# Kernel optimization log

Hardware: AMD Instinct MI355X
Metric: run time of the kernel (lower is better)

The kernel has to match this reference:

```python
import jax, jax.numpy as jnp
import numpy as np

N_ATOMS = 100000
N_EDGES = 800000
ATOM_FDIM = 133
HIDDEN = 256
DEPTH = 3
NUM_MOLS = 4096
BN_EPS = 1e-5


def setup_inputs() -> dict:
    key = jax.random.key(0)
    ks = jax.random.split(key, 16)
    f_atoms = jax.random.normal(ks[0], (N_ATOMS, ATOM_FDIM), dtype=jnp.float32)
    edge_index = jax.random.randint(ks[1], (2, N_EDGES), 0, N_ATOMS, dtype=jnp.int64)
    segment_ids = jnp.sort(jax.random.randint(ks[2], (N_ATOMS,), 0, NUM_MOLS, dtype=jnp.int64))
    s = 1.0 / np.sqrt(HIDDEN)
    return {
        "f_atoms": f_atoms,
        "W_in_w": jax.random.normal(ks[3], (ATOM_FDIM, HIDDEN), dtype=jnp.float32) / np.sqrt(ATOM_FDIM),
        "W_in_b": jnp.zeros((HIDDEN,), dtype=jnp.float32),
        "w1": jax.random.normal(ks[4], (DEPTH, HIDDEN, HIDDEN), dtype=jnp.float32) * s,
        "b1": jnp.zeros((DEPTH, HIDDEN), dtype=jnp.float32),
        "g1": jnp.ones((DEPTH, HIDDEN), dtype=jnp.float32),
        "be1": jnp.zeros((DEPTH, HIDDEN), dtype=jnp.float32),
        "w2": jax.random.normal(ks[5], (DEPTH, HIDDEN, HIDDEN), dtype=jnp.float32) * s,
        "b2": jnp.zeros((DEPTH, HIDDEN), dtype=jnp.float32),
        "g2": jnp.ones((DEPTH, HIDDEN), dtype=jnp.float32),
        "be2": jnp.zeros((DEPTH, HIDDEN), dtype=jnp.float32),
        "eps": jnp.zeros((DEPTH,), dtype=jnp.float32),
        "edge_index": edge_index,
        "segment_ids": segment_ids,
    }


def batchnorm(h, gamma, beta):
    # BatchNorm1d with batch statistics over the node dimension (training-mode math)
    mean = jnp.mean(h, axis=0)
    var = jnp.var(h, axis=0)
    return (h - mean) * jax.lax.rsqrt(var + BN_EPS) * gamma + beta


def reference(f_atoms, W_in_w, W_in_b, w1, b1, g1, be1, w2, b2, g2, be2, eps,
              edge_index, segment_ids):
    src, dst = edge_index[0], edge_index[1]
    x = jax.nn.relu(f_atoms @ W_in_w + W_in_b)  # [N, H]
    for i in range(DEPTH):
        agg = jnp.zeros_like(x).at[dst].add(x[src])  # gather + scatter-add
        h = agg + (1.0 + eps[i]) * x                 # epsilon self-term
        h = jax.nn.relu(batchnorm(h @ w1[i] + b1[i], g1[i], be1[i]))
        h = jax.nn.relu(batchnorm(h @ w2[i] + b2[i], g2[i], be2[i]))
        x = h  # dropout = identity (eval)
    sums = jax.ops.segment_sum(x, segment_ids, num_segments=NUM_MOLS)
    counts = jax.ops.segment_sum(jnp.ones((x.shape[0],), x.dtype), segment_ids,
                                 num_segments=NUM_MOLS)
    return sums / jnp.maximum(counts, 1.0)[:, None]  # per-molecule mean
```

## Files before the change

### kernel.cpp

```cpp
#include <hip/hip_runtime.h>
#include <hip/hip_bf16.h>

#define NA 100000
#define NE 800000
#define FDIM 133
#define KIN 192
#define H 256
#define NMOL 4096

typedef __attribute__((ext_vector_type(8))) short s16x8;
typedef __attribute__((ext_vector_type(4))) float f32x4;

__device__ __forceinline__ float bf2f(unsigned short h) {
    unsigned u = ((unsigned)h) << 16;
    return __builtin_bit_cast(float, u);
}
__device__ __forceinline__ unsigned short f2bf(float f) {
    unsigned u = __builtin_bit_cast(unsigned, f);
    u = u + 0x7FFFu + ((u >> 16) & 1u);
    return (unsigned short)(u >> 16);
}

__device__ __forceinline__ int swz(int row, int g) {
    return row * 64 + ((g ^ (row & 7)) << 3);
}

template<bool A_F32, bool AFFINE, bool RELU_OUT, bool STATS>
__global__ __launch_bounds__(256) void gemm_k(
    const void* __restrict__ Avoid,
    const unsigned short* __restrict__ BT,
    const float* __restrict__ bias,
    const float* __restrict__ aSc, const float* __restrict__ aSh,
    unsigned short* __restrict__ C,
    float* __restrict__ stSum, float* __restrict__ stSq,
    int M, int Kpad)
{
    __shared__ short lsA[128 * 64];
    __shared__ short lsB[128 * 64];
    __shared__ float lsSc[256], lsSh[256];
    __shared__ float lsS[128], lsQ[128];

    const int t = threadIdx.x;
    const int m0 = blockIdx.y * 128;
    const int n0 = blockIdx.x * 128;

    if (STATS && t < 128) { lsS[t] = 0.f; lsQ[t] = 0.f; }
    if (AFFINE) { lsSc[t] = aSc[t]; lsSh[t] = aSh[t]; }
    if (AFFINE) __syncthreads();

    const int sr = t >> 3;
    const int sg = t & 7;
    const int lane = t & 63;
    const int wid = t >> 6;
    const int wm = wid >> 1, wn = wid & 1;
    const int fr = lane & 15, fg = lane >> 4;

    f32x4 acc[4][4];
    #pragma unroll
    for (int i = 0; i < 4; i++)
        #pragma unroll
        for (int j = 0; j < 4; j++)
            acc[i][j] = f32x4{0.f, 0.f, 0.f, 0.f};

    const int nK = Kpad >> 6;
    s16x8 ra[4], rb[4];

    auto loadRegs = [&](int kc) {
        const int k0 = kc * 64;
        #pragma unroll
        for (int p = 0; p < 4; ++p) {
            int r = p * 32 + sr;
            int ga = m0 + r;
            if (A_F32) {
                const float* Af = (const float*)Avoid;
                s16x8 v;
                #pragma unroll
                for (int e = 0; e < 8; ++e) {
                    int k = k0 + sg * 8 + e;
                    float f = (ga < M && k < FDIM) ? Af[(size_t)ga * FDIM + k] : 0.f;
                    v[e] = (short)f2bf(f);
                }
                ra[p] = v;
            } else {
                const unsigned short* A = (const unsigned short*)Avoid;
                s16x8 z = {0,0,0,0,0,0,0,0};
                ra[p] = (ga < M) ? *(const s16x8*)(A + (size_t)ga * Kpad + k0 + sg * 8) : z;
            }
            rb[p] = *(const s16x8*)(BT + (size_t)(n0 + r) * Kpad + k0 + sg * 8);
        }
    };
    auto writeLds = [&](int kc) {
        const int k0 = kc * 64;
        #pragma unroll
        for (int p = 0; p < 4; ++p) {
            int r = p * 32 + sr;
            s16x8 va = ra[p];
            if (AFFINE) {
                #pragma unroll
                for (int e = 0; e < 8; ++e) {
                    int k = k0 + sg * 8 + e;
                    float f = bf2f((unsigned short)va[e]);
                    f = fmaxf(f * lsSc[k] + lsSh[k], 0.f);
                    va[e] = (short)f2bf(f);
                }
            }
            *(s16x8*)&lsA[swz(r, sg)] = va;
            *(s16x8*)&lsB[swz(r, sg)] = rb[p];
        }
    };

    loadRegs(0);
    for (int kc = 0; kc < nK; ++kc) {
        writeLds(kc);
        __syncthreads();
        if (kc + 1 < nK) loadRegs(kc + 1);
        #pragma unroll
        for (int ks = 0; ks < 2; ++ks) {
            s16x8 af[4], bg[4];
            #pragma unroll
            for (int mi = 0; mi < 4; ++mi)
                af[mi] = *(const s16x8*)&lsA[swz(wm * 64 + mi * 16 + fr, ks * 4 + fg)];
            #pragma unroll
            for (int ni = 0; ni < 4; ++ni)
                bg[ni] = *(const s16x8*)&lsB[swz(wn * 64 + ni * 16 + fr, ks * 4 + fg)];
            #pragma unroll
            for (int mi = 0; mi < 4; ++mi)
                #pragma unroll
                for (int ni = 0; ni < 4; ++ni)
                    acc[mi][ni] = __builtin_amdgcn_mfma_f32_16x16x32_bf16(
                        af[mi], bg[ni], acc[mi][ni], 0, 0, 0);
        }
        __syncthreads();
    }

    #pragma unroll
    for (int ni = 0; ni < 4; ++ni) {
        int lcol = wn * 64 + ni * 16 + fr;
        float bc = bias[n0 + lcol];
        float cs = 0.f, cq = 0.f;
        #pragma unroll
        for (int mi = 0; mi < 4; ++mi) {
            #pragma unroll
            for (int r = 0; r < 4; ++r) {
                int row = m0 + wm * 64 + mi * 16 + fg * 4 + r;
                if (row < M) {
                    float v = acc[mi][ni][r] + bc;
                    if (RELU_OUT) v = fmaxf(v, 0.f);
                    if (STATS) { cs += v; cq += v * v; }
                    C[(size_t)row * H + n0 + lcol] = f2bf(v);
                }
            }
        }
        if (STATS) {
            atomicAdd(&lsS[lcol], cs);
            atomicAdd(&lsQ[lcol], cq);
        }
    }
    if (STATS) {
        __syncthreads();
        if (t < 128) {
            atomicAdd(&stSum[n0 + t], lsS[t]);
            atomicAdd(&stSq[n0 + t], lsQ[t]);
        }
    }
}

__global__ void bnfin_k(float* __restrict__ sum, float* __restrict__ sumsq,
                        const float* __restrict__ g, const float* __restrict__ be,
                        float* __restrict__ scOut, float* __restrict__ shOut) {
    int c = threadIdx.x;
    float mean = sum[c] * (1.0f / NA);
    float var = sumsq[c] * (1.0f / NA) - mean * mean;
    float sc = g[c] * rsqrtf(var + 1e-5f);
    scOut[c] = sc;
    shOut[c] = be[c] - mean * sc;
    sum[c] = 0.f; sumsq[c] = 0.f;
}

__global__ void zero_k(int* __restrict__ counts, float* __restrict__ st, int* __restrict__ rowstart) {
    int i = blockIdx.x * 256 + threadIdx.x;
    if (i < NA) counts[i] = 0;
    if (blockIdx.x == 0) {
        st[threadIdx.x] = 0.f; st[threadIdx.x + 256] = 0.f;
        if (threadIdx.x == 0) rowstart[NA] = NE;
    }
}

__global__ void hist_k(const int* __restrict__ dst, int* __restrict__ counts) {
    int e = blockIdx.x * 256 + threadIdx.x;
    if (e < NE) atomicAdd(&counts[dst[e]], 1);
}
__global__ void scan1_k(const int* __restrict__ counts, int* __restrict__ excl, int* __restrict__ bsum) {
    __shared__ int sd[256];
    int i = blockIdx.x * 256 + threadIdx.x;
    int c = (i < NA) ? counts[i] : 0;
    sd[threadIdx.x] = c;
    __syncthreads();
    for (int off = 1; off < 256; off <<= 1) {
        int v = (threadIdx.x >= off) ? sd[threadIdx.x - off] : 0;
        __syncthreads();
        sd[threadIdx.x] += v;
        __syncthreads();
    }
    if (i < NA) excl[i] = sd[threadIdx.x] - c;
    if (threadIdx.x == 255) bsum[blockIdx.x] = sd[255];
}
__global__ void scan2_k(int* __restrict__ bsum, int nb) {
    __shared__ int sd[512];
    int t = threadIdx.x;
    int v = (t < nb) ? bsum[t] : 0;
    sd[t] = v;
    __syncthreads();
    for (int off = 1; off < 512; off <<= 1) {
        int u = (t >= off) ? sd[t - off] : 0;
        __syncthreads();
        sd[t] += u;
        __syncthreads();
    }
    if (t < nb) bsum[t] = sd[t] - v;
}
__global__ void scan3_k(int* __restrict__ rowstart, const int* __restrict__ bsum, int* __restrict__ cursor) {
    int i = blockIdx.x * 256 + threadIdx.x;
    if (i < NA) {
        int v = rowstart[i] + bsum[blockIdx.x];
        rowstart[i] = v;
        cursor[i] = v;
    }
}
__global__ void fill_k(const int* __restrict__ src, const int* __restrict__ dstArr,
                       int* __restrict__ cursor, int* __restrict__ esrc) {
    int e = blockIdx.x * 256 + threadIdx.x;
    if (e < NE) {
        int d = dstArr[e];
        int pos = atomicAdd(&cursor[d], 1);
        esrc[pos] = src[e];
    }
}

template<bool AFF>
__global__ __launch_bounds__(256) void agg_k(const unsigned short* __restrict__ X,
    const float* __restrict__ sc, const float* __restrict__ sh,
    const int* __restrict__ rowstart,
    const int* __restrict__ esrc, const float* __restrict__ epsArr, int layer,
    unsigned short* __restrict__ AGG)
{
    int wid = threadIdx.x >> 6, lane = threadIdx.x & 63;
    int row = blockIdx.x * 4 + wid;
    int half = lane >> 5;
    int c0 = (lane & 31) * 8;

    float s8[8], h8[8];
    if (AFF) {
        f32x4 a = *(const f32x4*)(sc + c0), b = *(const f32x4*)(sc + c0 + 4);
        f32x4 c = *(const f32x4*)(sh + c0), d = *(const f32x4*)(sh + c0 + 4);
        #pragma unroll
        for (int e = 0; e < 4; e++) { s8[e] = a[e]; s8[e + 4] = b[e]; h8[e] = c[e]; h8[e + 4] = d[e]; }
    }

    float a0[8] = {0,0,0,0,0,0,0,0}, a1[8] = {0,0,0,0,0,0,0,0};
    auto addv = [&](s16x8 u, float* a) {
        #pragma unroll
        for (int e = 0; e < 8; e++) {
            float f = bf2f((unsigned short)u[e]);
            if (AFF) f = fmaxf(f * s8[e] + h8[e], 0.f);
            a[e] += f;
        }
    };

    int s = rowstart[row], eEnd = rowstart[row + 1];
    int cnt = eEnd - s, mid = s + (cnt >> 1);
    int i = half ? mid : s;
    int end = half ? eEnd : mid;
    for (; i + 3 < end; i += 4) {
        int e0 = esrc[i], e1 = esrc[i + 1], e2 = esrc[i + 2], e3 = esrc[i + 3];
        s16x8 u0 = *(const s16x8*)(X + (size_t)e0 * H + c0);
        s16x8 u1 = *(const s16x8*)(X + (size_t)e1 * H + c0);
        s16x8 u2 = *(const s16x8*)(X + (size_t)e2 * H + c0);
        s16x8 u3 = *(const s16x8*)(X + (size_t)e3 * H + c0);
        addv(u0, a0); addv(u1, a1); addv(u2, a0); addv(u3, a1);
    }
    for (; i < end; ++i) {
        int e0 = esrc[i];
        s16x8 u = *(const s16x8*)(X + (size_t)e0 * H + c0);
        addv(u, a0);
    }

    if (half == 0) {
        float e1 = 1.0f + epsArr[layer];
        s16x8 u = *(const s16x8*)(X + (size_t)row * H + c0);
        #pragma unroll
        for (int e = 0; e < 8; e++) {
            float f = bf2f((unsigned short)u[e]);
            if (AFF) f = fmaxf(f * s8[e] + h8[e], 0.f);
            a0[e] += f * e1;
        }
    }

    s16x8 o;
    #pragma unroll
    for (int e = 0; e < 8; e++) {
        float tot = a0[e] + a1[e];
        tot += __shfl_xor(tot, 32);
        o[e] = (short)f2bf(tot);
    }
    if (half == 0)
        *(s16x8*)(AGG + (size_t)row * H + c0) = o;
}

__global__ void prep_all_k(const float* __restrict__ Win, const float* __restrict__ w1,
                           const float* __restrict__ w2, unsigned short* __restrict__ BTall) {
    int i = blockIdx.x * 256 + threadIdx.x;
    const int NIN = 256 * KIN;
    if (i < NIN) {
        int n = i / KIN, k = i % KIN;
        BTall[i] = (k < FDIM) ? f2bf(Win[(size_t)k * 256 + n]) : (unsigned short)0;
    } else if (i < NIN + 6 * 65536) {
        int j = i - NIN;
        int d = j >> 16, r = j & 65535;
        int n = r >> 8, k = r & 255;
        const float* W = (d & 1) ? w2 : w1;
        BTall[i] = f2bf(W[(size_t)(d >> 1) * 65536 + (size_t)k * 256 + n]);
    }
}

__global__ void molstart_k(const int* __restrict__ seg, int* __restrict__ ms) {
    int m = blockIdx.x * 256 + threadIdx.x;
    if (m <= NMOL) {
        int lo = 0, hi = NA;
        while (lo < hi) { int mid = (lo + hi) >> 1; if (seg[mid] < m) lo = mid + 1; else hi = mid; }
        ms[m] = lo;
    }
}
__global__ __launch_bounds__(64) void mean_k(const unsigned short* __restrict__ X,
    const float* __restrict__ sc, const float* __restrict__ sh,
    const int* __restrict__ ms, float* __restrict__ out)
{
    int m = blockIdx.x, lane = threadIdx.x;
    int half = lane >> 5;
    int c0 = (lane & 31) * 8;
    float s8[8], h8[8];
    {
        f32x4 a = *(const f32x4*)(sc + c0), b = *(const f32x4*)(sc + c0 + 4);
        f32x4 c = *(const f32x4*)(sh + c0), d = *(const f32x4*)(sh + c0 + 4);
        #pragma unroll
        for (int e = 0; e < 4; e++) { s8[e] = a[e]; s8[e + 4] = b[e]; h8[e] = c[e]; h8[e + 4] = d[e]; }
    }
    int a = ms[m], b = ms[m + 1];
    float acc[8] = {0,0,0,0,0,0,0,0};
    for (int r = a + half; r < b; r += 2) {
        s16x8 u = *(const s16x8*)(X + (size_t)r * H + c0);
        #pragma unroll
        for (int e = 0; e < 8; e++)
            acc[e] += fmaxf(bf2f((unsigned short)u[e]) * s8[e] + h8[e], 0.f);
    }
    float inv = (b > a) ? 1.0f / (float)(b - a) : 0.0f;
    f32x4 o0, o1;
    #pragma unroll
    for (int e = 0; e < 8; e++) {
        float tot = acc[e] + __shfl_xor(acc[e], 32);
        tot *= inv;
        if (e < 4) o0[e] = tot; else o1[e - 4] = tot;
    }
    if (half == 0) {
        *(f32x4*)(out + (size_t)m * H + c0) = o0;
        *(f32x4*)(out + (size_t)m * H + c0 + 4) = o1;
    }
}

extern "C" void kernel_launch(void* const* d_in, const int* in_sizes, int n_in,
                              void* d_out, int out_size, void* d_ws, size_t ws_size,
                              hipStream_t stream) {
    const float* f_atoms = (const float*)d_in[0];
    const float* W_in_w  = (const float*)d_in[1];
    const float* W_in_b  = (const float*)d_in[2];
    const float* w1  = (const float*)d_in[3];
    const float* b1  = (const float*)d_in[4];
    const float* g1  = (const float*)d_in[5];
    const float* be1 = (const float*)d_in[6];
    const float* w2  = (const float*)d_in[7];
    const float* b2  = (const float*)d_in[8];
    const float* g2  = (const float*)d_in[9];
    const float* be2 = (const float*)d_in[10];
    const float* epsArr = (const float*)d_in[11];
    const int* edge = (const int*)d_in[12];
    const int* seg  = (const int*)d_in[13];
    float* out = (float*)d_out;

    char* w = (char*)d_ws;
    size_t off = 0;
    auto alloc = [&](size_t bytes) {
        char* p = w + off;
        off = (off + bytes + 255) & ~(size_t)255;
        return p;
    };
    unsigned short* X   = (unsigned short*)alloc((size_t)NA * H * 2);
    unsigned short* AGG = (unsigned short*)alloc((size_t)NA * H * 2);
    unsigned short* T1  = (unsigned short*)alloc((size_t)NA * H * 2);
    unsigned short* BTall = (unsigned short*)alloc(((size_t)256 * KIN + 6 * 65536) * 2);
    float* stSum = (float*)alloc(256 * 4);
    float* stSq  = (float*)alloc(256 * 4);
    float* sc1 = (float*)alloc(256 * 4);
    float* sh1 = (float*)alloc(256 * 4);
    float* sc2 = (float*)alloc(256 * 4);
    float* sh2 = (float*)alloc(256 * 4);
    int* counts   = (int*)alloc((size_t)NA * 4);
    int* rowstart = (int*)alloc((size_t)(NA + 1) * 4);
    int* cursor   = (int*)alloc((size_t)NA * 4);
    int* esrc     = (int*)alloc((size_t)NE * 4);
    int* bsum     = (int*)alloc(512 * 4);
    int* ms       = (int*)alloc((NMOL + 1) * 4);

    unsigned short* BTin = BTall;
    unsigned short* BT1[3], *BT2[3];
    for (int d = 0; d < 3; ++d) {
        BT1[d] = BTall + 256 * KIN + (size_t)(2 * d) * 65536;
        BT2[d] = BTall + 256 * KIN + (size_t)(2 * d + 1) * 65536;
    }

    const int* esrcIn = edge;
    const int* edst   = edge + NE;

    zero_k<<<(NA + 255) / 256, 256, 0, stream>>>(counts, stSum, rowstart);
    prep_all_k<<<(256 * KIN + 6 * 65536 + 255) / 256, 256, 0, stream>>>(W_in_w, w1, w2, BTall);

    hist_k<<<(NE + 255) / 256, 256, 0, stream>>>(edst, counts);
    scan1_k<<<391, 256, 0, stream>>>(counts, rowstart, bsum);
    scan2_k<<<1, 512, 0, stream>>>(bsum, 391);
    scan3_k<<<391, 256, 0, stream>>>(rowstart, bsum, cursor);
    fill_k<<<(NE + 255) / 256, 256, 0, stream>>>(esrcIn, edst, cursor, esrc);
    molstart_k<<<(NMOL + 256) / 256, 256, 0, stream>>>(seg, ms);

    gemm_k<true, false, true, false><<<dim3(2, (NA + 127) / 128), 256, 0, stream>>>(
        f_atoms, BTin, W_in_b, nullptr, nullptr, X, nullptr, nullptr, NA, KIN);

    for (int d = 0; d < 3; ++d) {
        if (d == 0)
            agg_k<false><<<NA / 4, 256, 0, stream>>>(X, nullptr, nullptr,
                rowstart, esrc, epsArr, d, AGG);
        else
            agg_k<true><<<NA / 4, 256, 0, stream>>>(X, sc2, sh2,
                rowstart, esrc, epsArr, d, AGG);
        gemm_k<false, false, false, true><<<dim3(2, (NA + 127) / 128), 256, 0, stream>>>(
            AGG, BT1[d], b1 + d * 256, nullptr, nullptr, T1, stSum, stSq, NA, 256);
        bnfin_k<<<1, 256, 0, stream>>>(stSum, stSq, g1 + d * 256, be1 + d * 256, sc1, sh1);
        gemm_k<false, true, false, true><<<dim3(2, (NA + 127) / 128), 256, 0, stream>>>(
            T1, BT2[d], b2 + d * 256, sc1, sh1, X, stSum, stSq, NA, 256);
        bnfin_k<<<1, 256, 0, stream>>>(stSum, stSq, g2 + d * 256, be2 + d * 256, sc2, sh2);
    }

    mean_k<<<NMOL, 64, 0, stream>>>(X, sc2, sh2, ms, out);
}
```

Before: 785.4 us.

## Widen GEMM tile to full 256 output columns with 512-thread blocks

After: 838.4 us. 6.7% more time.

```diff
diff --git a/kernel.cpp b/kernel.cpp
--- a/kernel.cpp
+++ b/kernel.cpp
@@ -26,7 +26,7 @@
 }
 
 template<bool A_F32, bool AFFINE, bool RELU_OUT, bool STATS>
-__global__ __launch_bounds__(256) void gemm_k(
+__global__ __launch_bounds__(512, 4) void gemm_k(
     const void* __restrict__ Avoid,
     const unsigned short* __restrict__ BT,
     const float* __restrict__ bias,
@@ -36,24 +36,23 @@
     int M, int Kpad)
 {
     __shared__ short lsA[128 * 64];
-    __shared__ short lsB[128 * 64];
+    __shared__ short lsB[256 * 64];
     __shared__ float lsSc[256], lsSh[256];
-    __shared__ float lsS[128], lsQ[128];
+    __shared__ float lsS[256], lsQ[256];
 
     const int t = threadIdx.x;
-    const int m0 = blockIdx.y * 128;
-    const int n0 = blockIdx.x * 128;
-
-    if (STATS && t < 128) { lsS[t] = 0.f; lsQ[t] = 0.f; }
-    if (AFFINE) { lsSc[t] = aSc[t]; lsSh[t] = aSh[t]; }
+    const int m0 = blockIdx.x * 128;
+
+    if (STATS && t < 256) { lsS[t] = 0.f; lsQ[t] = 0.f; }
+    if (AFFINE && t < 256) { lsSc[t] = aSc[t]; lsSh[t] = aSh[t]; }
     if (AFFINE) __syncthreads();
 
-    const int sr = t >> 3;
-    const int sg = t & 7;
     const int lane = t & 63;
     const int wid = t >> 6;
-    const int wm = wid >> 1, wn = wid & 1;
+    const int wm = wid >> 2, wn = wid & 3;
     const int fr = lane & 15, fg = lane >> 4;
+    const int srow = t >> 3;
+    const int sg = t & 7;
 
     f32x4 acc[4][4];
     #pragma unroll
@@ -63,13 +62,13 @@
             acc[i][j] = f32x4{0.f, 0.f, 0.f, 0.f};
 
     const int nK = Kpad >> 6;
-    s16x8 ra[4], rb[4];
+    s16x8 ra[2], rb[4];
 
     auto loadRegs = [&](int kc) {
         const int k0 = kc * 64;
         #pragma unroll
-        for (int p = 0; p < 4; ++p) {
-            int r = p * 32 + sr;
+        for (int p = 0; p < 2; ++p) {
+            int r = srow + p * 64;
             int ga = m0 + r;
             if (A_F32) {
                 const float* Af = (const float*)Avoid;
@@ -86,14 +85,15 @@
                 s16x8 z = {0,0,0,0,0,0,0,0};
                 ra[p] = (ga < M) ? *(const s16x8*)(A + (size_t)ga * Kpad + k0 + sg * 8) : z;
             }
-            rb[p] = *(const s16x8*)(BT + (size_t)(n0 + r) * Kpad + k0 + sg * 8);
-        }
+        }
+        #pragma unroll
+        for (int p = 0; p < 4; ++p)
+            rb[p] = *(const s16x8*)(BT + (size_t)(srow + p * 64) * Kpad + k0 + sg * 8);
     };
     auto writeLds = [&](int kc) {
         const int k0 = kc * 64;
         #pragma unroll
-        for (int p = 0; p < 4; ++p) {
-            int r = p * 32 + sr;
+        for (int p = 0; p < 2; ++p) {
             s16x8 va = ra[p];
             if (AFFINE) {
                 #pragma unroll
@@ -104,9 +104,11 @@
                     va[e] = (short)f2bf(f);
                 }
             }
-            *(s16x8*)&lsA[swz(r, sg)] = va;
-            *(s16x8*)&lsB[swz(r, sg)] = rb[p];
-        }
+            *(s16x8*)&lsA[swz(srow + p * 64, sg)] = va;
+        }
+        #pragma unroll
+        for (int p = 0; p < 4; ++p)
+            *(s16x8*)&lsB[swz(srow + p * 64, sg)] = rb[p];
     };
 
     loadRegs(0);
@@ -136,7 +138,7 @@
     #pragma unroll
     for (int ni = 0; ni < 4; ++ni) {
         int lcol = wn * 64 + ni * 16 + fr;
-        float bc = bias[n0 + lcol];
+        float bc = bias[lcol];
         float cs = 0.f, cq = 0.f;
         #pragma unroll
         for (int mi = 0; mi < 4; ++mi) {
@@ -147,7 +149,7 @@
                     float v = acc[mi][ni][r] + bc;
                     if (RELU_OUT) v = fmaxf(v, 0.f);
                     if (STATS) { cs += v; cq += v * v; }
-                    C[(size_t)row * H + n0 + lcol] = f2bf(v);
+                    C[(size_t)row * H + lcol] = f2bf(v);
                 }
             }
         }
@@ -158,9 +160,9 @@
     }
     if (STATS) {
         __syncthreads();
-        if (t < 128) {
-            atomicAdd(&stSum[n0 + t], lsS[t]);
-            atomicAdd(&stSq[n0 + t], lsQ[t]);
+        if (t < 256) {
+            atomicAdd(&stSum[t], lsS[t]);
+            atomicAdd(&stSq[t], lsQ[t]);
         }
     }
 }
@@ -430,7 +432,9 @@
     fill_k<<<(NE + 255) / 256, 256, 0, stream>>>(esrcIn, edst, cursor, esrc);
     molstart_k<<<(NMOL + 256) / 256, 256, 0, stream>>>(seg, ms);
 
-    gemm_k<true, false, true, false><<<dim3(2, (NA + 127) / 128), 256, 0, stream>>>(
+    const int GB = (NA + 127) / 128;
+
+    gemm_k<true, false, true, false><<<GB, 512, 0, stream>>>(
         f_atoms, BTin, W_in_b, nullptr, nullptr, X, nullptr, nullptr, NA, KIN);
 
     for (int d = 0; d < 3; ++d) {
@@ -440,10 +444,10 @@
         else
             agg_k<true><<<NA / 4, 256, 0, stream>>>(X, sc2, sh2,
                 rowstart, esrc, epsArr, d, AGG);
-        gemm_k<false, false, false, true><<<dim3(2, (NA + 127) / 128), 256, 0, stream>>>(
+        gemm_k<false, false, false, true><<<GB, 512, 0, stream>>>(
             AGG, BT1[d], b1 + d * 256, nullptr, nullptr, T1, stSum, stSq, NA, 256);
         bnfin_k<<<1, 256, 0, stream>>>(stSum, stSq, g1 + d * 256, be1 + d * 256, sc1, sh1);
-        gemm_k<false, true, false, true><<<dim3(2, (NA + 127) / 128), 256, 0, stream>>>(
+        gemm_k<false, true, false, true><<<GB, 512, 0, stream>>>(
             T1, BT2[d], b2 + d * 256, sc1, sh1, X, stSum, stSq, NA, 256);
         bnfin_k<<<1, 256, 0, stream>>>(stSum, stSq, g2 + d * 256, be2 + d * 256, sc2, sh2);
     }
```

## Restructure GEMM with direct global-to-LDS double buffering and staged epilogue

Applied to the files above, without the earlier changes.

New measurement: 827.0 us. 1.05x slower.

```diff
diff --git a/kernel.cpp b/kernel.cpp
--- a/kernel.cpp
+++ b/kernel.cpp
@@ -10,6 +10,7 @@
 
 typedef __attribute__((ext_vector_type(8))) short s16x8;
 typedef __attribute__((ext_vector_type(4))) float f32x4;
+typedef __attribute__((ext_vector_type(4))) unsigned int u32x4;
 
 __device__ __forceinline__ float bf2f(unsigned short h) {
     unsigned u = ((unsigned)h) << 16;
@@ -20,14 +21,21 @@
     u = u + 0x7FFFu + ((u >> 16) & 1u);
     return (unsigned short)(u >> 16);
 }
+__device__ __forceinline__ void nt_store16(s16x8 v, void* p) {
+    __builtin_nontemporal_store(__builtin_bit_cast(u32x4, v), (u32x4*)p);
+}
 
 __device__ __forceinline__ int swz(int row, int g) {
     return row * 64 + ((g ^ (row & 7)) << 3);
 }
-
-template<bool A_F32, bool AFFINE, bool RELU_OUT, bool STATS>
-__global__ __launch_bounds__(256) void gemm_k(
-    const void* __restrict__ Avoid,
+__device__ __forceinline__ void gload_lds16(const void* g, void* l) {
+    __builtin_amdgcn_global_load_lds((const __attribute__((address_space(1))) unsigned int*)g,
+                                     (__attribute__((address_space(3))) unsigned int*)l, 16, 0, 0);
+}
+
+template<bool AFFINE, bool RELU_OUT, bool STATS>
+__global__ __launch_bounds__(256, 3) void gemm_k(
+    const unsigned short* __restrict__ A,
     const unsigned short* __restrict__ BT,
     const float* __restrict__ bias,
     const float* __restrict__ aSc, const float* __restrict__ aSh,
@@ -35,120 +43,108 @@
     float* __restrict__ stSum, float* __restrict__ stSq,
     int M, int Kpad)
 {
-    __shared__ short lsA[128 * 64];
-    __shared__ short lsB[128 * 64];
-    __shared__ float lsSc[256], lsSh[256];
-    __shared__ float lsS[128], lsQ[128];
+    __shared__ short lsA[2][64 * 64];
+    __shared__ short lsB[2][128 * 64];
 
     const int t = threadIdx.x;
-    const int m0 = blockIdx.y * 128;
+    const int m0 = blockIdx.y * 64;
     const int n0 = blockIdx.x * 128;
 
-    if (STATS && t < 128) { lsS[t] = 0.f; lsQ[t] = 0.f; }
-    if (AFFINE) { lsSc[t] = aSc[t]; lsSh[t] = aSh[t]; }
-    if (AFFINE) __syncthreads();
-
-    const int sr = t >> 3;
-    const int sg = t & 7;
-    const int lane = t & 63;
-    const int wid = t >> 6;
+    const int lane = t & 63, wid = t >> 6;
     const int wm = wid >> 1, wn = wid & 1;
     const int fr = lane & 15, fg = lane >> 4;
 
-    f32x4 acc[4][4];
+    auto stage = [&](int kc, int b) {
+        #pragma unroll
+        for (int c = 0; c < 2; ++c) {
+            int sb = c * 256 + wid * 64;
+            int slot = sb + lane;
+            int row = slot >> 3, gs = slot & 7;
+            int coff = kc * 64 + ((gs ^ (row & 7)) << 3);
+            int rowA = m0 + row; if (rowA > M - 1) rowA = M - 1;
+            gload_lds16(A + (size_t)rowA * Kpad + coff, &lsA[b][sb * 8]);
+        }
+        #pragma unroll
+        for (int c = 0; c < 4; ++c) {
+            int sb = c * 256 + wid * 64;
+            int slot = sb + lane;
+            int row = slot >> 3, gs = slot & 7;
+            int coff = kc * 64 + ((gs ^ (row & 7)) << 3);
+            gload_lds16(BT + (size_t)(n0 + row) * Kpad + coff, &lsB[b][sb * 8]);
+        }
+    };
+
+    f32x4 acc[2][4];
     #pragma unroll
-    for (int i = 0; i < 4; i++)
+    for (int i = 0; i < 2; i++)
         #pragma unroll
         for (int j = 0; j < 4; j++)
             acc[i][j] = f32x4{0.f, 0.f, 0.f, 0.f};
 
     const int nK = Kpad >> 6;
-    s16x8 ra[4], rb[4];
-
-    auto loadRegs = [&](int kc) {
-        const int k0 = kc * 64;
-        #pragma unroll
-        for (int p = 0; p < 4; ++p) {
-            int r = p * 32 + sr;
-            int ga = m0 + r;
-            if (A_F32) {
-                const float* Af = (const float*)Avoid;
-                s16x8 v;
+
+    stage(0, 0);
+    __syncthreads();
+    int buf = 0;
+    for (int kc = 0; kc < nK; ++kc) {
+        if (kc + 1 < nK) stage(kc + 1, buf ^ 1);
+        #pragma unroll
+        for (int ks = 0; ks < 2; ++ks) {
+            s16x8 af[2], bg[4];
+            #pragma unroll
+            for (int mi = 0; mi < 2; ++mi)
+                af[mi] = *(const s16x8*)&lsA[buf][swz(wm * 32 + mi * 16 + fr, ks * 4 + fg)];
+            #pragma unroll
+            for (int ni = 0; ni < 4; ++ni)
+                bg[ni] = *(const s16x8*)&lsB[buf][swz(wn * 64 + ni * 16 + fr, ks * 4 + fg)];
+            if (AFFINE) {
+                int kb = kc * 64 + ks * 32 + fg * 8;
+                f32x4 s0 = *(const f32x4*)&aSc[kb], s1 = *(const f32x4*)&aSc[kb + 4];
+                f32x4 h0 = *(const f32x4*)&aSh[kb], h1 = *(const f32x4*)&aSh[kb + 4];
                 #pragma unroll
-                for (int e = 0; e < 8; ++e) {
-                    int k = k0 + sg * 8 + e;
-                    float f = (ga < M && k < FDIM) ? Af[(size_t)ga * FDIM + k] : 0.f;
-                    v[e] = (short)f2bf(f);
-                }
-                ra[p] = v;
-            } else {
-                const unsigned short* A = (const unsigned short*)Avoid;
-                s16x8 z = {0,0,0,0,0,0,0,0};
-                ra[p] = (ga < M) ? *(const s16x8*)(A + (size_t)ga * Kpad + k0 + sg * 8) : z;
-            }
-            rb[p] = *(const s16x8*)(BT + (size_t)(n0 + r) * Kpad + k0 + sg * 8);
-        }
-    };
-    auto writeLds = [&](int kc) {
-        const int k0 = kc * 64;
-        #pragma unroll
-        for (int p = 0; p < 4; ++p) {
-            int r = p * 32 + sr;
-            s16x8 va = ra[p];
-            if (AFFINE) {
-                #pragma unroll
-                for (int e = 0; e < 8; ++e) {
-                    int k = k0 + sg * 8 + e;
-                    float f = bf2f((unsigned short)va[e]);
-                    f = fmaxf(f * lsSc[k] + lsSh[k], 0.f);
-                    va[e] = (short)f2bf(f);
+                for (int mi = 0; mi < 2; ++mi) {
+                    s16x8 v = af[mi];
+                    #pragma unroll
+                    for (int e = 0; e < 4; ++e) {
+                        float f0 = fmaxf(bf2f((unsigned short)v[e]) * s0[e] + h0[e], 0.f);
+                        float f1 = fmaxf(bf2f((unsigned short)v[e + 4]) * s1[e] + h1[e], 0.f);
+                        v[e] = (short)f2bf(f0);
+                        v[e + 4] = (short)f2bf(f1);
+                    }
+                    af[mi] = v;
                 }
             }
-            *(s16x8*)&lsA[swz(r, sg)] = va;
-            *(s16x8*)&lsB[swz(r, sg)] = rb[p];
-        }
-    };
-
-    loadRegs(0);
-    for (int kc = 0; kc < nK; ++kc) {
-        writeLds(kc);
-        __syncthreads();
-        if (kc + 1 < nK) loadRegs(kc + 1);
-        #pragma unroll
-        for (int ks = 0; ks < 2; ++ks) {
-            s16x8 af[4], bg[4];
             #pragma unroll
-            for (int mi = 0; mi < 4; ++mi)
-                af[mi] = *(const s16x8*)&lsA[swz(wm * 64 + mi * 16 + fr, ks * 4 + fg)];
-            #pragma unroll
-            for (int ni = 0; ni < 4; ++ni)
-                bg[ni] = *(const s16x8*)&lsB[swz(wn * 64 + ni * 16 + fr, ks * 4 + fg)];
-            #pragma unroll
-            for (int mi = 0; mi < 4; ++mi)
+            for (int mi = 0; mi < 2; ++mi)
                 #pragma unroll
                 for (int ni = 0; ni < 4; ++ni)
                     acc[mi][ni] = __builtin_amdgcn_mfma_f32_16x16x32_bf16(
                         af[mi], bg[ni], acc[mi][ni], 0, 0, 0);
         }
         __syncthreads();
-    }
-
+        buf ^= 1;
+    }
+
+    float* lsS = (float*)&lsA[0][0];
+    float* lsQ = lsS + 128;
+    short* cst = &lsB[0][0];
+    const int CST = 136;
+    if (STATS && t < 128) { lsS[t] = 0.f; lsQ[t] = 0.f; }
+    __syncthreads();
     #pragma unroll
     for (int ni = 0; ni < 4; ++ni) {
         int lcol = wn * 64 + ni * 16 + fr;
         float bc = bias[n0 + lcol];
         float cs = 0.f, cq = 0.f;
         #pragma unroll
-        for (int mi = 0; mi < 4; ++mi) {
+        for (int mi = 0; mi < 2; ++mi) {
             #pragma unroll
             for (int r = 0; r < 4; ++r) {
-                int row = m0 + wm * 64 + mi * 16 + fg * 4 + r;
-                if (row < M) {
-                    float v = acc[mi][ni][r] + bc;
-                    if (RELU_OUT) v = fmaxf(v, 0.f);
-                    if (STATS) { cs += v; cq += v * v; }
-                    C[(size_t)row * H + n0 + lcol] = f2bf(v);
-                }
+                int rl = wm * 32 + mi * 16 + fg * 4 + r;
+                float v = acc[mi][ni][r] + bc;
+                if (RELU_OUT) v = fmaxf(v, 0.f);
+                if (STATS && (m0 + rl < M)) { cs += v; cq += v * v; }
+                cst[rl * CST + lcol] = (short)f2bf(v);
             }
         }
         if (STATS) {
@@ -156,12 +152,19 @@
             atomicAdd(&lsQ[lcol], cq);
         }
     }
-    if (STATS) {
-        __syncthreads();
-        if (t < 128) {
-            atomicAdd(&stSum[n0 + t], lsS[t]);
-            atomicAdd(&stSq[n0 + t], lsQ[t]);
-        }
+    __syncthreads();
+    #pragma unroll
+    for (int p = 0; p < 4; ++p) {
+        int idx = p * 256 + t;
+        int rl = idx >> 4;
+        int col = (idx & 15) * 8;
+        int row = m0 + rl;
+        if (row < M)
+            nt_store16(*(const s16x8*)&cst[rl * CST + col], C + (size_t)row * H + n0 + col);
+    }
+    if (STATS && t < 128) {
+        atomicAdd(&stSum[n0 + t], lsS[t]);
+        atomicAdd(&stSq[n0 + t], lsQ[t]);
     }
 }
 
@@ -183,6 +186,14 @@
     if (blockIdx.x == 0) {
         st[threadIdx.x] = 0.f; st[threadIdx.x + 256] = 0.f;
         if (threadIdx.x == 0) rowstart[NA] = NE;
+    }
+}
+
+__global__ void cast_fa_k(const float* __restrict__ fa, unsigned short* __restrict__ FA) {
+    long long i = (long long)blockIdx.x * 256 + threadIdx.x;
+    if (i < (long long)NA * KIN) {
+        int r = (int)(i / KIN), k = (int)(i % KIN);
+        FA[i] = (k < FDIM) ? f2bf(fa[(size_t)r * FDIM + k]) : (unsigned short)0;
     }
 }
 
@@ -304,7 +315,7 @@
         o[e] = (short)f2bf(tot);
     }
     if (half == 0)
-        *(s16x8*)(AGG + (size_t)row * H + c0) = o;
+        nt_store16(o, AGG + (size_t)row * H + c0);
 }
 
 __global__ void prep_all_k(const float* __restrict__ Win, const float* __restrict__ w1,
@@ -396,6 +407,7 @@
     unsigned short* X   = (unsigned short*)alloc((size_t)NA * H * 2);
     unsigned short* AGG = (unsigned short*)alloc((size_t)NA * H * 2);
     unsigned short* T1  = (unsigned short*)alloc((size_t)NA * H * 2);
+    unsigned short* FA  = T1;
     unsigned short* BTall = (unsigned short*)alloc(((size_t)256 * KIN + 6 * 65536) * 2);
     float* stSum = (float*)alloc(256 * 4);
     float* stSq  = (float*)alloc(256 * 4);
@@ -422,6 +434,7 @@
 
     zero_k<<<(NA + 255) / 256, 256, 0, stream>>>(counts, stSum, rowstart);
     prep_all_k<<<(256 * KIN + 6 * 65536 + 255) / 256, 256, 0, stream>>>(W_in_w, w1, w2, BTall);
+    cast_fa_k<<<(int)(((long long)NA * KIN + 255) / 256), 256, 0, stream>>>(f_atoms, FA);
 
     hist_k<<<(NE + 255) / 256, 256, 0, stream>>>(edst, counts);
     scan1_k<<<391, 256, 0, stream>>>(counts, rowstart, bsum);
@@ -430,8 +443,10 @@
     fill_k<<<(NE + 255) / 256, 256, 0, stream>>>(esrcIn, edst, cursor, esrc);
     molstart_k<<<(NMOL + 256) / 256, 256, 0, stream>>>(seg, ms);
 
-    gemm_k<true, false, true, false><<<dim3(2, (NA + 127) / 128), 256, 0, stream>>>(
-        f_atoms, BTin, W_in_b, nullptr, nullptr, X, nullptr, nullptr, NA, KIN);
+    const dim3 GB(2, (NA + 63) / 64);
+
+    gemm_k<false, true, false><<<GB, 256, 0, stream>>>(
+        FA, BTin, W_in_b, nullptr, nullptr, X, nullptr, nullptr, NA, KIN);
 
     for (int d = 0; d < 3; ++d) {
         if (d == 0)
@@ -440,10 +455,10 @@
         else
             agg_k<true><<<NA / 4, 256, 0, stream>>>(X, sc2, sh2,
                 rowstart, esrc, epsArr, d, AGG);
-        gemm_k<false, false, false, true><<<dim3(2, (NA + 127) / 128), 256, 0, stream>>>(
+        gemm_k<false, false, true><<<GB, 256, 0, stream>>>(
             AGG, BT1[d], b1 + d * 256, nullptr, nullptr, T1, stSum, stSq, NA, 256);
         bnfin_k<<<1, 256, 0, stream>>>(stSum, stSq, g1 + d * 256, be1 + d * 256, sc1, sh1);
-        gemm_k<false, true, false, true><<<dim3(2, (NA + 127) / 128), 256, 0, stream>>>(
+        gemm_k<true, false, true><<<GB, 256, 0, stream>>>(
             T1, BT2[d], b2 + d * 256, sc1, sh1, X, stSum, stSq, NA, 256);
         bnfin_k<<<1, 256, 0, stream>>>(stSum, stSq, g2 + d * 256, be2 + d * 256, sc2, sh2);
     }
```
